# Performance work log

Measured on AMD Instinct MI355X. Metric: run time of the kernel, lower is better.

The kernel has to match this reference:

```python
import jax, jax.numpy as jnp
import numpy as np
import math

H = 768          # bert hidden size
N_HYPO = 384     # number of hyponym instance embeddings
N_HYPER = 384    # number of hypernym instance embeddings
NUM_LABELS = 3


def setup_inputs() -> dict:
    key = jax.random.key(0)
    k1, k2, k3 = jax.random.split(key, 3)
    return {
        "hypo_embeddings": jax.random.normal(k1, (N_HYPO, H), dtype=jnp.float32),
        "hyper_embeddings": jax.random.normal(k2, (N_HYPER, H), dtype=jnp.float32),
        "W_cls": jax.random.normal(k3, (NUM_LABELS, 4 * H), dtype=jnp.float32) * 0.02,
        "b_cls": jnp.zeros((NUM_LABELS,), dtype=jnp.float32),
    }


def reference(hypo_embeddings, hyper_embeddings, W_cls, b_cls):
    h = hypo_embeddings.shape[-1]
    inv_sqrt_h = 1.0 / math.sqrt(h)
    # elementwise outer-product attention score: tanh(x_i * y_j) summed over hidden
    # [n_hypo, n_hyper, h] intermediate -> [n_hypo, n_hyper]
    att = jnp.tanh(hypo_embeddings[:, None, :] * hyper_embeddings[None, :, :]).sum(-1) * inv_sqrt_h

    hypo_side_att = jax.nn.softmax(att, axis=-1)   # rows attend over hypers
    hyper_side_att = jax.nn.softmax(att, axis=0)   # cols attend over hypos

    hyper_typ = hypo_side_att.sum(axis=0)
    hyper_typ = hyper_typ / hyper_typ.sum()
    hypo_typ = hyper_side_att.sum(axis=-1)
    hypo_typ = hypo_typ / hypo_typ.sum()

    # typicalness-weighted prototype pooling
    hyper_prototype = jnp.einsum('nm,md,n->d', hypo_side_att, hyper_embeddings, hypo_typ)
    hypo_prototype = jnp.einsum('nm,nd,m->d', hyper_side_att, hypo_embeddings, hyper_typ)

    feats = jnp.concatenate([
        hyper_prototype,
        hypo_prototype,
        hyper_prototype - hypo_prototype,
        hyper_prototype * hypo_prototype,
    ])  # [4h]
    sub_pred = W_cls @ feats + b_cls  # [num_labels]
    return sub_pred
```

## Files before the change

kernel.cpp:

```cpp
#include <hip/hip_runtime.h>

#define NN 384
#define HH 768
#define HP 772
#define L2E 1.4426950408889634f
#define TWO_L2E 2.8853900817779268f
#define INV_SQRT_H 0.03608439182435161f
#define ATT_L2E (INV_SQRT_H * L2E)

__device__ __forceinline__ float exp2_hw(float x) { return __builtin_amdgcn_exp2f(x); }
__device__ __forceinline__ float rcp_hw(float x) { return __builtin_amdgcn_rcpf(x); }

#define WS_E(ws)      ((ws))
#define WS_ET(ws)     ((ws) + NN * NN)
#define WS_ROWP(ws)   ((ws) + 2 * NN * NN)
#define WS_COLP(ws)   ((ws) + 2 * NN * NN + 48 * NN)
#define WS_ROWRS(ws)  ((ws) + 2 * NN * NN + 96 * NN)
#define WS_COLRS(ws)  (WS_ROWRS(ws) + NN)
#define WS_HYPERT(ws) (WS_COLRS(ws) + NN)
#define WS_HYPOT(ws)  (WS_HYPERT(ws) + NN)
#define WS_WHYPER(ws) (WS_HYPOT(ws) + NN)
#define WS_WHYPO(ws)  (WS_WHYPER(ws) + NN)

__global__ __launch_bounds__(256) void k_att(const float* __restrict__ X,
                                             const float* __restrict__ Y,
                                             float* __restrict__ ws,
                                             float* __restrict__ out) {
    __shared__ float smem[16 * HP + 256];
    float* xs = smem;
    float* ys = smem + 8 * HP;
    float* part = smem + 16 * HP;
    float* E = WS_E(ws);
    float* ET = WS_ET(ws);
    float* rowP = WS_ROWP(ws);
    float* colP = WS_COLP(ws);

    const int tid = threadIdx.x;
    const int tt = blockIdx.x;
    const int it = tt / 48, jt = tt - it * 48;
    const int i0 = it * 8, j0 = jt * 8;

    if (tt == 0 && tid < 3) out[tid] = 0.f;

    const float4* gx = (const float4*)(X + i0 * HH);
    const float4* gy = (const float4*)(Y + j0 * HH);
#pragma unroll
    for (int p = 0; p < 6; p++) {
        int e = tid + p * 256;
        int r = e / 192, c = e - r * 192;
        float4 vx = gx[e];
        float4 vy = gy[e];
        ((float4*)(xs + r * HP))[c] = vx;
        vy.x *= TWO_L2E; vy.y *= TWO_L2E; vy.z *= TWO_L2E; vy.w *= TWO_L2E;
        ((float4*)(ys + r * HP))[c] = vy;
    }
    __syncthreads();

    const int wv = tid >> 6, ln = tid & 63;
    const int i = ln >> 3, j = ln & 7;
    const float4* xr = (const float4*)(xs + i * HP) + wv * 48;
    const float4* yr = (const float4*)(ys + j * HP) + wv * 48;
    float a0 = 0.f, a1 = 0.f, a2 = 0.f, a3 = 0.f;
#pragma unroll 8
    for (int m = 0; m < 48; m++) {
        float4 a = xr[m];
        float4 b = yr[m];
        a0 += rcp_hw(exp2_hw(a.x * b.x) + 1.f);
        a1 += rcp_hw(exp2_hw(a.y * b.y) + 1.f);
        a2 += rcp_hw(exp2_hw(a.z * b.z) + 1.f);
        a3 += rcp_hw(exp2_hw(a.w * b.w) + 1.f);
    }
    part[wv * 64 + ln] = (a0 + a1) + (a2 + a3);
    __syncthreads();
    if (tid < 64) {
        float s = part[tid] + part[64 + tid] + part[128 + tid] + part[192 + tid];
        float ev = exp2_hw((768.f - 2.f * s) * ATT_L2E);
        int ii = tid >> 3, jj = tid & 7;
        E[(i0 + ii) * NN + (j0 + jj)] = ev;
        ET[(j0 + jj) * NN + (i0 + ii)] = ev;
        float rs = ev;
        rs += __shfl_xor(rs, 1, 64); rs += __shfl_xor(rs, 2, 64); rs += __shfl_xor(rs, 4, 64);
        if (jj == 0) rowP[jt * NN + i0 + ii] = rs;
        float cs = ev;
        cs += __shfl_xor(cs, 8, 64); cs += __shfl_xor(cs, 16, 64); cs += __shfl_xor(cs, 32, 64);
        if (ii == 0) colP[it * NN + j0 + jj] = cs;
    }
}

__global__ __launch_bounds__(256) void k_typ(float* __restrict__ ws) {
    __shared__ float red[4];
    const int b = blockIdx.x, tid = threadIdx.x;
    const float* E = WS_E(ws);
    const float* ET = WS_ET(ws);
    const bool isCol = b < NN;
    const int x = isCol ? b : b - NN;
    const float* P = isCol ? WS_ROWP(ws) : WS_COLP(ws);
    const float* M = isCol ? ET : E;

    float s1 = 0.f, s2 = 0.f;
#pragma unroll 8
    for (int k = 0; k < 48; k++) {
        s1 += P[k * NN + tid];
        if (tid < 128) s2 += P[k * NN + tid + 256];
    }
    float r1 = rcp_hw(s1);
    float acc = M[x * NN + tid] * r1;
    float r2 = 0.f;
    if (tid < 128) {
        r2 = rcp_hw(s2);
        acc += M[x * NN + tid + 256] * r2;
    }
    if (isCol ? (b == 0) : (b == NN)) {
        float* RS = isCol ? WS_ROWRS(ws) : WS_COLRS(ws);
        RS[tid] = r1;
        if (tid < 128) RS[tid + 256] = r2;
    }
#pragma unroll
    for (int o = 32; o; o >>= 1) acc += __shfl_xor(acc, o, 64);
    if ((tid & 63) == 0) red[tid >> 6] = acc;
    __syncthreads();
    if (tid == 0) {
        float S = (red[0] + red[1]) + (red[2] + red[3]);
        (isCol ? WS_HYPERT(ws) : WS_HYPOT(ws))[x] = S * (1.f / NN);
    }
}

__global__ __launch_bounds__(256) void k_w(float* __restrict__ ws) {
    __shared__ float red[4];
    const int b = blockIdx.x, tid = threadIdx.x;
    const float* E = WS_E(ws);
    const float* ET = WS_ET(ws);
    const bool isCol = b < NN;
    const int x = isCol ? b : b - NN;
    const float* M = isCol ? ET : E;
    const float* RS = isCol ? WS_ROWRS(ws) : WS_COLRS(ws);
    const float* T = isCol ? WS_HYPOT(ws) : WS_HYPERT(ws);

    float acc = M[x * NN + tid] * RS[tid] * T[tid];
    if (tid < 128) acc += M[x * NN + tid + 256] * RS[tid + 256] * T[tid + 256];
#pragma unroll
    for (int o = 32; o; o >>= 1) acc += __shfl_xor(acc, o, 64);
    if ((tid & 63) == 0) red[tid >> 6] = acc;
    __syncthreads();
    if (tid == 0) (isCol ? WS_WHYPER(ws) : WS_WHYPO(ws))[x] = (red[0] + red[1]) + (red[2] + red[3]);
}

__global__ __launch_bounds__(256) void k_pc(const float* __restrict__ X,
                                            const float* __restrict__ Y,
                                            const float* __restrict__ W,
                                            const float* __restrict__ bias,
                                            const float* __restrict__ ws,
                                            float* __restrict__ out) {
    __shared__ float red[2][4][64];
    __shared__ float hp_s[64], hq_s[64];
    const int tid = threadIdx.x, bb = blockIdx.x;
    const int dl = tid & 63, w = tid >> 6;
    const int d = bb * 64 + dl;
    const float* w_hyper = WS_WHYPER((float*)ws);
    const float* w_hypo  = WS_WHYPO((float*)ws);

    float sp = 0.f, sq = 0.f;
    for (int j = w * 96; j < w * 96 + 96; j++) {
        sp += w_hyper[j] * Y[j * HH + d];
        sq += w_hypo[j]  * X[j * HH + d];
    }
    red[0][w][dl] = sp;
    red[1][w][dl] = sq;
    __syncthreads();
    if (tid < 64) {
        hp_s[tid] = red[0][0][tid] + red[0][1][tid] + red[0][2][tid] + red[0][3][tid];
        hq_s[tid] = red[1][0][tid] + red[1][1][tid] + red[1][2][tid] + red[1][3][tid];
    }
    __syncthreads();

    float acc = 0.f;
    if (tid < 192) {
        const int c = tid >> 6;
        const float hp = hp_s[dl], hq = hq_s[dl];
        const int base = c * 3072 + bb * 64 + dl;
        acc = W[base] * hp + W[base + 768] * hq + W[base + 1536] * (hp - hq)
            + W[base + 2304] * (hp * hq);
    }
#pragma unroll
    for (int o = 32; o; o >>= 1) acc += __shfl_xor(acc, o, 64);
    if (tid < 192 && (tid & 63) == 0) atomicAdd(out + (tid >> 6), acc);
    if (bb == 0 && tid < 3) atomicAdd(out + tid, bias[tid]);
}

extern "C" void kernel_launch(void* const* d_in, const int* in_sizes, int n_in,
                              void* d_out, int out_size, void* d_ws, size_t ws_size,
                              hipStream_t stream) {
    const float* X = (const float*)d_in[0];
    const float* Y = (const float*)d_in[1];
    const float* W = (const float*)d_in[2];
    const float* B = (const float*)d_in[3];
    float* out = (float*)d_out;
    float* ws = (float*)d_ws;

    k_att<<<2304, 256, 0, stream>>>(X, Y, ws, out);
    k_typ<<<768, 256, 0, stream>>>(ws);
    k_w<<<768, 256, 0, stream>>>(ws);
    k_pc<<<12, 256, 0, stream>>>(X, Y, W, B, ws, out);
}
```

Measured before the change: 111.7 us.

## Batch sigmoid reciprocals in attention loop and restructure prototype pooling kernels

The inner attention loop now clamps the exponent and combines four sigmoid terms over a single shared reciprocal, cutting the number of transcendental rcp instructions roughly fourfold at the cost of extra multiplies. The weight and prototype stages are fused into one kernel where each block computes eight weights and accumulates weighted embedding rows atomically, replacing the narrow 12-block pooling kernel. A single-block classifier kernel then writes the output directly, so the atomic output accumulation goes away. The clamp is there to avoid overflow in the combined product, and the atomics make the prototype sums nondeterministic in order.

```diff
diff --git a/kernel.cpp b/kernel.cpp
--- a/kernel.cpp
+++ b/kernel.cpp
@@ -7,6 +7,7 @@
 #define TWO_L2E 2.8853900817779268f
 #define INV_SQRT_H 0.03608439182435161f
 #define ATT_L2E (INV_SQRT_H * L2E)
+#define TCLAMP 25.0f
 
 __device__ __forceinline__ float exp2_hw(float x) { return __builtin_amdgcn_exp2f(x); }
 __device__ __forceinline__ float rcp_hw(float x) { return __builtin_amdgcn_rcpf(x); }
@@ -19,13 +20,12 @@
 #define WS_COLRS(ws)  (WS_ROWRS(ws) + NN)
 #define WS_HYPERT(ws) (WS_COLRS(ws) + NN)
 #define WS_HYPOT(ws)  (WS_HYPERT(ws) + NN)
-#define WS_WHYPER(ws) (WS_HYPOT(ws) + NN)
-#define WS_WHYPO(ws)  (WS_WHYPER(ws) + NN)
+#define WS_HP(ws)     (WS_HYPOT(ws) + NN)
+#define WS_HQ(ws)     (WS_HP(ws) + HH)
 
 __global__ __launch_bounds__(256) void k_att(const float* __restrict__ X,
                                              const float* __restrict__ Y,
-                                             float* __restrict__ ws,
-                                             float* __restrict__ out) {
+                                             float* __restrict__ ws) {
     __shared__ float smem[16 * HP + 256];
     float* xs = smem;
     float* ys = smem + 8 * HP;
@@ -40,8 +40,6 @@
     const int it = tt / 48, jt = tt - it * 48;
     const int i0 = it * 8, j0 = jt * 8;
 
-    if (tt == 0 && tid < 3) out[tid] = 0.f;
-
     const float4* gx = (const float4*)(X + i0 * HH);
     const float4* gy = (const float4*)(Y + j0 * HH);
 #pragma unroll
@@ -60,21 +58,28 @@
     const int i = ln >> 3, j = ln & 7;
     const float4* xr = (const float4*)(xs + i * HP) + wv * 48;
     const float4* yr = (const float4*)(ys + j * HP) + wv * 48;
-    float a0 = 0.f, a1 = 0.f, a2 = 0.f, a3 = 0.f;
+    float s = 0.f;
 #pragma unroll 8
     for (int m = 0; m < 48; m++) {
-        float4 a = xr[m];
-        float4 b = yr[m];
-        a0 += rcp_hw(exp2_hw(a.x * b.x) + 1.f);
-        a1 += rcp_hw(exp2_hw(a.y * b.y) + 1.f);
-        a2 += rcp_hw(exp2_hw(a.z * b.z) + 1.f);
-        a3 += rcp_hw(exp2_hw(a.w * b.w) + 1.f);
-    }
-    part[wv * 64 + ln] = (a0 + a1) + (a2 + a3);
+        float4 a4 = xr[m];
+        float4 b4 = yr[m];
+        float t0 = fminf(a4.x * b4.x, TCLAMP);
+        float t1 = fminf(a4.y * b4.y, TCLAMP);
+        float t2 = fminf(a4.z * b4.z, TCLAMP);
+        float t3 = fminf(a4.w * b4.w, TCLAMP);
+        float pa = exp2_hw(t0) + 1.f;
+        float pb = exp2_hw(t1) + 1.f;
+        float pc = exp2_hw(t2) + 1.f;
+        float pd = exp2_hw(t3) + 1.f;
+        float ab = pa * pb, cd = pc * pd;
+        float num = (pa + pb) * cd + (pc + pd) * ab;
+        s = fmaf(num, rcp_hw(ab * cd), s);
+    }
+    part[wv * 64 + ln] = s;
     __syncthreads();
     if (tid < 64) {
-        float s = part[tid] + part[64 + tid] + part[128 + tid] + part[192 + tid];
-        float ev = exp2_hw((768.f - 2.f * s) * ATT_L2E);
+        float t = part[tid] + part[64 + tid] + part[128 + tid] + part[192 + tid];
+        float ev = exp2_hw((768.f - 2.f * t) * ATT_L2E);
         int ii = tid >> 3, jj = tid & 7;
         E[(i0 + ii) * NN + (j0 + jj)] = ev;
         ET[(j0 + jj) * NN + (i0 + ii)] = ev;
@@ -97,6 +102,12 @@
     const float* P = isCol ? WS_ROWP(ws) : WS_COLP(ws);
     const float* M = isCol ? ET : E;
 
+    if (b == 1) {
+        float* pz = WS_HP(ws);
+#pragma unroll
+        for (int q = 0; q < 6; q++) pz[tid + q * 256] = 0.f;
+    }
+
     float s1 = 0.f, s2 = 0.f;
 #pragma unroll 8
     for (int k = 0; k < 48; k++) {
@@ -125,66 +136,70 @@
     }
 }
 
-__global__ __launch_bounds__(256) void k_w(float* __restrict__ ws) {
+__global__ __launch_bounds__(256) void k_wp(const float* __restrict__ X,
+                                            const float* __restrict__ Y,
+                                            float* __restrict__ ws) {
     __shared__ float red[4];
-    const int b = blockIdx.x, tid = threadIdx.x;
-    const float* E = WS_E(ws);
-    const float* ET = WS_ET(ws);
-    const bool isCol = b < NN;
-    const int x = isCol ? b : b - NN;
-    const float* M = isCol ? ET : E;
-    const float* RS = isCol ? WS_ROWRS(ws) : WS_COLRS(ws);
-    const float* T = isCol ? WS_HYPOT(ws) : WS_HYPERT(ws);
-
-    float acc = M[x * NN + tid] * RS[tid] * T[tid];
-    if (tid < 128) acc += M[x * NN + tid + 256] * RS[tid + 256] * T[tid + 256];
-#pragma unroll
-    for (int o = 32; o; o >>= 1) acc += __shfl_xor(acc, o, 64);
-    if ((tid & 63) == 0) red[tid >> 6] = acc;
-    __syncthreads();
-    if (tid == 0) (isCol ? WS_WHYPER(ws) : WS_WHYPO(ws))[x] = (red[0] + red[1]) + (red[2] + red[3]);
-}
-
-__global__ __launch_bounds__(256) void k_pc(const float* __restrict__ X,
-                                            const float* __restrict__ Y,
-                                            const float* __restrict__ W,
-                                            const float* __restrict__ bias,
-                                            const float* __restrict__ ws,
-                                            float* __restrict__ out) {
-    __shared__ float red[2][4][64];
-    __shared__ float hp_s[64], hq_s[64];
-    const int tid = threadIdx.x, bb = blockIdx.x;
-    const int dl = tid & 63, w = tid >> 6;
-    const int d = bb * 64 + dl;
-    const float* w_hyper = WS_WHYPER((float*)ws);
-    const float* w_hypo  = WS_WHYPO((float*)ws);
-
-    float sp = 0.f, sq = 0.f;
-    for (int j = w * 96; j < w * 96 + 96; j++) {
-        sp += w_hyper[j] * Y[j * HH + d];
-        sq += w_hypo[j]  * X[j * HH + d];
-    }
-    red[0][w][dl] = sp;
-    red[1][w][dl] = sq;
-    __syncthreads();
-    if (tid < 64) {
-        hp_s[tid] = red[0][0][tid] + red[0][1][tid] + red[0][2][tid] + red[0][3][tid];
-        hq_s[tid] = red[1][0][tid] + red[1][1][tid] + red[1][2][tid] + red[1][3][tid];
-    }
-    __syncthreads();
-
-    float acc = 0.f;
-    if (tid < 192) {
-        const int c = tid >> 6;
-        const float hp = hp_s[dl], hq = hq_s[dl];
-        const int base = c * 3072 + bb * 64 + dl;
-        acc = W[base] * hp + W[base + 768] * hq + W[base + 1536] * (hp - hq)
-            + W[base + 2304] * (hp * hq);
-    }
-#pragma unroll
-    for (int o = 32; o; o >>= 1) acc += __shfl_xor(acc, o, 64);
-    if (tid < 192 && (tid & 63) == 0) atomicAdd(out + (tid >> 6), acc);
-    if (bb == 0 && tid < 3) atomicAdd(out + tid, bias[tid]);
+    const int bb = blockIdx.x, tid = threadIdx.x;
+    const bool hyperSide = bb < 48;
+    const int jbase = (hyperSide ? bb : bb - 48) * 8;
+    const float* M  = hyperSide ? WS_ET(ws) : WS_E(ws);
+    const float* RS = hyperSide ? WS_ROWRS(ws) : WS_COLRS(ws);
+    const float* T  = hyperSide ? WS_HYPOT(ws) : WS_HYPERT(ws);
+    const float* V  = hyperSide ? Y : X;
+    float* proto    = hyperSide ? WS_HP(ws) : WS_HQ(ws);
+
+    float p0 = 0.f, p1 = 0.f, p2 = 0.f;
+#pragma unroll
+    for (int q = 0; q < 8; q++) {
+        const int jj = jbase + q;
+        float acc = M[jj * NN + tid] * RS[tid] * T[tid];
+        if (tid < 128) acc += M[jj * NN + tid + 256] * RS[tid + 256] * T[tid + 256];
+#pragma unroll
+        for (int o = 32; o; o >>= 1) acc += __shfl_xor(acc, o, 64);
+        if ((tid & 63) == 0) red[tid >> 6] = acc;
+        __syncthreads();
+        const float wj = (red[0] + red[1]) + (red[2] + red[3]);
+        p0 = fmaf(wj, V[jj * HH + tid], p0);
+        p1 = fmaf(wj, V[jj * HH + tid + 256], p1);
+        p2 = fmaf(wj, V[jj * HH + tid + 512], p2);
+        __syncthreads();
+    }
+    atomicAdd(proto + tid, p0);
+    atomicAdd(proto + tid + 256, p1);
+    atomicAdd(proto + tid + 512, p2);
+}
+
+__global__ __launch_bounds__(256) void k_cls(const float* __restrict__ W,
+                                             const float* __restrict__ bias,
+                                             const float* __restrict__ ws,
+                                             float* __restrict__ out) {
+    __shared__ float red[3][4];
+    const int t = threadIdx.x;
+    const float* hp = WS_HP((float*)ws);
+    const float* hq = WS_HQ((float*)ws);
+    float acc0 = 0.f, acc1 = 0.f, acc2 = 0.f;
+    for (int d = t; d < 4 * HH; d += 256) {
+        int seg = d / HH, r = d - seg * HH;
+        float f = (seg == 0) ? hp[r] : (seg == 1) ? hq[r] : (seg == 2) ? (hp[r] - hq[r]) : (hp[r] * hq[r]);
+        acc0 += W[d] * f;
+        acc1 += W[3072 + d] * f;
+        acc2 += W[6144 + d] * f;
+    }
+#pragma unroll
+    for (int o = 32; o; o >>= 1) {
+        acc0 += __shfl_xor(acc0, o, 64);
+        acc1 += __shfl_xor(acc1, o, 64);
+        acc2 += __shfl_xor(acc2, o, 64);
+    }
+    if ((t & 63) == 0) {
+        red[0][t >> 6] = acc0;
+        red[1][t >> 6] = acc1;
+        red[2][t >> 6] = acc2;
+    }
+    __syncthreads();
+    if (t < 3)
+        out[t] = red[t][0] + red[t][1] + red[t][2] + red[t][3] + bias[t];
 }
 
 extern "C" void kernel_launch(void* const* d_in, const int* in_sizes, int n_in,
@@ -197,8 +212,8 @@
     float* out = (float*)d_out;
     float* ws = (float*)d_ws;
 
-    k_att<<<2304, 256, 0, stream>>>(X, Y, ws, out);
+    k_att<<<2304, 256, 0, stream>>>(X, Y, ws);
     k_typ<<<768, 256, 0, stream>>>(ws);
-    k_w<<<768, 256, 0, stream>>>(ws);
-    k_pc<<<12, 256, 0, stream>>>(X, Y, W, B, ws, out);
-}
+    k_wp<<<96, 256, 0, stream>>>(X, Y, ws);
+    k_cls<<<1, 256, 0, stream>>>(W, B, ws, out);
+}
```

After: 116.3 us. +4.1%, slower.

## Fuse typicalness, weighting, pooling and classifier into one grid-synchronized kernel

Applied to the files above, without the earlier changes.

Merges k_typ, k_w and k_pc into a single kernel that uses an atomic counter spin barrier between the typicalness phase and the weighting phase. Each block keeps its reciprocal row/column sums in registers and accumulates its weighted embedding row into the prototypes with atomics. The last block to finish computes the classifier output. This removes two kernel launches and the workspace round trips for RS and the weights. In exchange it depends on all 768 blocks being co-resident for the spin barrier, and it adds heavy float atomic traffic on the prototype buffers.

```diff
diff --git a/kernel.cpp b/kernel.cpp
--- a/kernel.cpp
+++ b/kernel.cpp
@@ -10,22 +10,23 @@
 
 __device__ __forceinline__ float exp2_hw(float x) { return __builtin_amdgcn_exp2f(x); }
 __device__ __forceinline__ float rcp_hw(float x) { return __builtin_amdgcn_rcpf(x); }
+__device__ __forceinline__ float atomic_ld(const float* p) {
+    return __hip_atomic_load(p, __ATOMIC_RELAXED, __HIP_MEMORY_SCOPE_AGENT);
+}
 
 #define WS_E(ws)      ((ws))
 #define WS_ET(ws)     ((ws) + NN * NN)
 #define WS_ROWP(ws)   ((ws) + 2 * NN * NN)
 #define WS_COLP(ws)   ((ws) + 2 * NN * NN + 48 * NN)
-#define WS_ROWRS(ws)  ((ws) + 2 * NN * NN + 96 * NN)
-#define WS_COLRS(ws)  (WS_ROWRS(ws) + NN)
-#define WS_HYPERT(ws) (WS_COLRS(ws) + NN)
+#define WS_HYPERT(ws) ((ws) + 2 * NN * NN + 96 * NN)
 #define WS_HYPOT(ws)  (WS_HYPERT(ws) + NN)
-#define WS_WHYPER(ws) (WS_HYPOT(ws) + NN)
-#define WS_WHYPO(ws)  (WS_WHYPER(ws) + NN)
+#define WS_HP(ws)     (WS_HYPOT(ws) + NN)
+#define WS_HQ(ws)     (WS_HP(ws) + HH)
+#define WS_CNT(ws)    ((unsigned int*)(WS_HQ(ws) + HH))
 
 __global__ __launch_bounds__(256) void k_att(const float* __restrict__ X,
                                              const float* __restrict__ Y,
-                                             float* __restrict__ ws,
-                                             float* __restrict__ out) {
+                                             float* __restrict__ ws) {
     __shared__ float smem[16 * HP + 256];
     float* xs = smem;
     float* ys = smem + 8 * HP;
@@ -40,7 +41,12 @@
     const int it = tt / 48, jt = tt - it * 48;
     const int i0 = it * 8, j0 = jt * 8;
 
-    if (tt == 0 && tid < 3) out[tid] = 0.f;
+    if (tt == 0) {
+        float* pz = WS_HP(ws);
+#pragma unroll
+        for (int q = 0; q < 6; q++) pz[tid + q * 256] = 0.f;
+        if (tid == 0) { WS_CNT(ws)[0] = 0u; WS_CNT(ws)[1] = 0u; }
+    }
 
     const float4* gx = (const float4*)(X + i0 * HH);
     const float4* gy = (const float4*)(Y + j0 * HH);
@@ -87,15 +93,24 @@
     }
 }
 
-__global__ __launch_bounds__(256) void k_typ(float* __restrict__ ws) {
+__global__ __launch_bounds__(256) void k_rest(const float* __restrict__ X,
+                                              const float* __restrict__ Y,
+                                              const float* __restrict__ W,
+                                              const float* __restrict__ bias,
+                                              float* __restrict__ ws,
+                                              float* __restrict__ out) {
     __shared__ float red[4];
+    __shared__ float redc[3][4];
+    __shared__ int lastFlag;
+    __shared__ float hps[HH], hqs[HH];
     const int b = blockIdx.x, tid = threadIdx.x;
+    const bool isCol = b < NN;
+    const int x = isCol ? b : b - NN;
     const float* E = WS_E(ws);
     const float* ET = WS_ET(ws);
-    const bool isCol = b < NN;
-    const int x = isCol ? b : b - NN;
     const float* P = isCol ? WS_ROWP(ws) : WS_COLP(ws);
     const float* M = isCol ? ET : E;
+    unsigned int* cnt = WS_CNT(ws);
 
     float s1 = 0.f, s2 = 0.f;
 #pragma unroll 8
@@ -104,17 +119,9 @@
         if (tid < 128) s2 += P[k * NN + tid + 256];
     }
     float r1 = rcp_hw(s1);
+    float r2 = (tid < 128) ? rcp_hw(s2) : 0.f;
     float acc = M[x * NN + tid] * r1;
-    float r2 = 0.f;
-    if (tid < 128) {
-        r2 = rcp_hw(s2);
-        acc += M[x * NN + tid + 256] * r2;
-    }
-    if (isCol ? (b == 0) : (b == NN)) {
-        float* RS = isCol ? WS_ROWRS(ws) : WS_COLRS(ws);
-        RS[tid] = r1;
-        if (tid < 128) RS[tid + 256] = r2;
-    }
+    if (tid < 128) acc += M[x * NN + tid + 256] * r2;
 #pragma unroll
     for (int o = 32; o; o >>= 1) acc += __shfl_xor(acc, o, 64);
     if ((tid & 63) == 0) red[tid >> 6] = acc;
@@ -122,69 +129,67 @@
     if (tid == 0) {
         float S = (red[0] + red[1]) + (red[2] + red[3]);
         (isCol ? WS_HYPERT(ws) : WS_HYPOT(ws))[x] = S * (1.f / NN);
-    }
-}
-
-__global__ __launch_bounds__(256) void k_w(float* __restrict__ ws) {
-    __shared__ float red[4];
-    const int b = blockIdx.x, tid = threadIdx.x;
-    const float* E = WS_E(ws);
-    const float* ET = WS_ET(ws);
-    const bool isCol = b < NN;
-    const int x = isCol ? b : b - NN;
-    const float* M = isCol ? ET : E;
-    const float* RS = isCol ? WS_ROWRS(ws) : WS_COLRS(ws);
-    const float* T = isCol ? WS_HYPOT(ws) : WS_HYPERT(ws);
-
-    float acc = M[x * NN + tid] * RS[tid] * T[tid];
-    if (tid < 128) acc += M[x * NN + tid + 256] * RS[tid + 256] * T[tid + 256];
-#pragma unroll
-    for (int o = 32; o; o >>= 1) acc += __shfl_xor(acc, o, 64);
-    if ((tid & 63) == 0) red[tid >> 6] = acc;
-    __syncthreads();
-    if (tid == 0) (isCol ? WS_WHYPER(ws) : WS_WHYPO(ws))[x] = (red[0] + red[1]) + (red[2] + red[3]);
-}
-
-__global__ __launch_bounds__(256) void k_pc(const float* __restrict__ X,
-                                            const float* __restrict__ Y,
-                                            const float* __restrict__ W,
-                                            const float* __restrict__ bias,
-                                            const float* __restrict__ ws,
-                                            float* __restrict__ out) {
-    __shared__ float red[2][4][64];
-    __shared__ float hp_s[64], hq_s[64];
-    const int tid = threadIdx.x, bb = blockIdx.x;
-    const int dl = tid & 63, w = tid >> 6;
-    const int d = bb * 64 + dl;
-    const float* w_hyper = WS_WHYPER((float*)ws);
-    const float* w_hypo  = WS_WHYPO((float*)ws);
-
-    float sp = 0.f, sq = 0.f;
-    for (int j = w * 96; j < w * 96 + 96; j++) {
-        sp += w_hyper[j] * Y[j * HH + d];
-        sq += w_hypo[j]  * X[j * HH + d];
-    }
-    red[0][w][dl] = sp;
-    red[1][w][dl] = sq;
-    __syncthreads();
-    if (tid < 64) {
-        hp_s[tid] = red[0][0][tid] + red[0][1][tid] + red[0][2][tid] + red[0][3][tid];
-        hq_s[tid] = red[1][0][tid] + red[1][1][tid] + red[1][2][tid] + red[1][3][tid];
-    }
-    __syncthreads();
-
-    float acc = 0.f;
-    if (tid < 192) {
-        const int c = tid >> 6;
-        const float hp = hp_s[dl], hq = hq_s[dl];
-        const int base = c * 3072 + bb * 64 + dl;
-        acc = W[base] * hp + W[base + 768] * hq + W[base + 1536] * (hp - hq)
-            + W[base + 2304] * (hp * hq);
-    }
-#pragma unroll
-    for (int o = 32; o; o >>= 1) acc += __shfl_xor(acc, o, 64);
-    if (tid < 192 && (tid & 63) == 0) atomicAdd(out + (tid >> 6), acc);
-    if (bb == 0 && tid < 3) atomicAdd(out + tid, bias[tid]);
+        __threadfence();
+        __hip_atomic_fetch_add(&cnt[0], 1u, __ATOMIC_ACQ_REL, __HIP_MEMORY_SCOPE_AGENT);
+        while (__hip_atomic_load(&cnt[0], __ATOMIC_ACQUIRE, __HIP_MEMORY_SCOPE_AGENT) < 768u)
+            __builtin_amdgcn_s_sleep(2);
+    }
+    __syncthreads();
+
+    const float* Tv = isCol ? WS_HYPOT(ws) : WS_HYPERT(ws);
+    float acc2 = M[x * NN + tid] * r1 * atomic_ld(Tv + tid);
+    if (tid < 128) acc2 += M[x * NN + tid + 256] * r2 * atomic_ld(Tv + tid + 256);
+#pragma unroll
+    for (int o = 32; o; o >>= 1) acc2 += __shfl_xor(acc2, o, 64);
+    if ((tid & 63) == 0) red[tid >> 6] = acc2;
+    __syncthreads();
+    const float wj = (red[0] + red[1]) + (red[2] + red[3]);
+    const float* V = isCol ? Y : X;
+    float* proto = isCol ? WS_HP(ws) : WS_HQ(ws);
+    atomicAdd(proto + tid,       wj * V[x * HH + tid]);
+    atomicAdd(proto + tid + 256, wj * V[x * HH + tid + 256]);
+    atomicAdd(proto + tid + 512, wj * V[x * HH + tid + 512]);
+
+    __threadfence();
+    __syncthreads();
+    if (tid == 0) {
+        unsigned int old = __hip_atomic_fetch_add(&cnt[1], 1u, __ATOMIC_ACQ_REL,
+                                                  __HIP_MEMORY_SCOPE_AGENT);
+        lastFlag = (old == 767u);
+    }
+    __syncthreads();
+    if (!lastFlag) return;
+
+#pragma unroll
+    for (int q = 0; q < 3; q++) {
+        hps[tid + q * 256] = atomic_ld(WS_HP(ws) + tid + q * 256);
+        hqs[tid + q * 256] = atomic_ld(WS_HQ(ws) + tid + q * 256);
+    }
+    __syncthreads();
+
+    float a0 = 0.f, a1 = 0.f, a2 = 0.f;
+    for (int d = tid; d < 4 * HH; d += 256) {
+        int seg = d / HH, r = d - seg * HH;
+        float hpv = hps[r], hqv = hqs[r];
+        float f = (seg == 0) ? hpv : (seg == 1) ? hqv : (seg == 2) ? (hpv - hqv) : (hpv * hqv);
+        a0 += W[d] * f;
+        a1 += W[3072 + d] * f;
+        a2 += W[6144 + d] * f;
+    }
+#pragma unroll
+    for (int o = 32; o; o >>= 1) {
+        a0 += __shfl_xor(a0, o, 64);
+        a1 += __shfl_xor(a1, o, 64);
+        a2 += __shfl_xor(a2, o, 64);
+    }
+    if ((tid & 63) == 0) {
+        redc[0][tid >> 6] = a0;
+        redc[1][tid >> 6] = a1;
+        redc[2][tid >> 6] = a2;
+    }
+    __syncthreads();
+    if (tid < 3)
+        out[tid] = redc[tid][0] + redc[tid][1] + redc[tid][2] + redc[tid][3] + bias[tid];
 }
 
 extern "C" void kernel_launch(void* const* d_in, const int* in_sizes, int n_in,
@@ -197,8 +202,6 @@
     float* out = (float*)d_out;
     float* ws = (float*)d_ws;
 
-    k_att<<<2304, 256, 0, stream>>>(X, Y, ws, out);
-    k_typ<<<768, 256, 0, stream>>>(ws);
-    k_w<<<768, 256, 0, stream>>>(ws);
-    k_pc<<<12, 256, 0, stream>>>(X, Y, W, B, ws, out);
-}
+    k_att<<<2304, 256, 0, stream>>>(X, Y, ws);
+    k_rest<<<768, 256, 0, stream>>>(X, Y, W, B, ws, out);
+}
```

After: 205.3 us. +83.8%, slower.
